# Kernel tuning notes

Measured on AMD Instinct MI355X. Metric: run time of the kernel, lower is better.

The kernel has to match this reference:

```python
import jax, jax.numpy as jnp
import numpy as np


def _gru(x, w_ih, w_hh, b_ih, b_hh):
    # x: [B, T, D]; torch nn.GRU (batch_first) semantics, h0 = 0
    B = x.shape[0]
    H = w_hh.shape[1]
    def step(h, xt):
        gi = xt @ w_ih.T + b_ih          # [B, 3H]
        gh = h @ w_hh.T + b_hh           # [B, 3H]
        ir, iz, inn = jnp.split(gi, 3, axis=-1)
        hr, hz, hn = jnp.split(gh, 3, axis=-1)
        r = jax.nn.sigmoid(ir + hr)
        z = jax.nn.sigmoid(iz + hz)
        n = jnp.tanh(inn + r * hn)
        h_new = (1.0 - z) * n + z * h
        return h_new, h_new
    h0 = jnp.zeros((B, H), x.dtype)
    _, ys = jax.lax.scan(step, h0, jnp.swapaxes(x, 0, 1))
    return jnp.swapaxes(ys, 0, 1)        # [B, T, H]


def setup_inputs() -> dict:
    key = jax.random.key(0)
    ks = iter(jax.random.split(key, 40))
    def p(shape, scale=0.05):
        return jax.random.normal(next(ks), shape, dtype=jnp.float32) * scale
    B, T, Z, S = 1024, 2, 100, 6
    return {
        "x": p((B, T, Z, S), 1.0),
        # actor: GRU(6 -> 64) + SimpleSubActor(64 -> 512 -> 128 -> 1)
        "a_gru_wih": p((192, 6)), "a_gru_whh": p((192, 64)),
        "a_gru_bih": p((192,)), "a_gru_bhh": p((192,)),
        "a_fc1_w": p((512, 64)), "a_fc1_b": p((512,)),
        "a_fc2_w": p((128, 512)), "a_fc2_b": p((128,)),
        "a_fc3_w": p((1, 128)), "a_fc3_b": p((1,)),
        # critic: GRU(35 -> 32) + SimpleSubCritic(32 -> 512 -> 256 -> 1)
        "c_gru_wih": p((96, 35)), "c_gru_whh": p((96, 32)),
        "c_gru_bih": p((96,)), "c_gru_bhh": p((96,)),
        "c_fc1_w": p((512, 32)), "c_fc1_b": p((512,)),
        "c_fc2_w": p((256, 512)), "c_fc2_b": p((256,)),
        "c_fc3_w": p((1, 256)), "c_fc3_b": p((1,)),
        # LocalizedModule(35 -> 512 -> 256 -> 1)
        "lm_fc1_w": p((512, 35)), "lm_fc1_b": p((512,)),
        "lm_fc2_w": p((256, 512)), "lm_fc2_b": p((256,)),
        "lm_fc3_w": p((1, 256)), "lm_fc3_b": p((1,)),
    }


def reference(x, a_gru_wih, a_gru_whh, a_gru_bih, a_gru_bhh,
              a_fc1_w, a_fc1_b, a_fc2_w, a_fc2_b, a_fc3_w, a_fc3_b,
              c_gru_wih, c_gru_whh, c_gru_bih, c_gru_bhh,
              c_fc1_w, c_fc1_b, c_fc2_w, c_fc2_b, c_fc3_w, c_fc3_b,
              lm_fc1_w, lm_fc1_b, lm_fc2_w, lm_fc2_b, lm_fc3_w, lm_fc3_b):
    B, T, Z, S = x.shape
    # ---- SimpleActor: same GRU+MLP shared across zones -> batch zones ----
    # torch: a[i] from x[:, :, i]; torch.stack(a) -> [Z, B, T, 1], then .view(-1, T, Z)
    xz = jnp.transpose(x, (2, 0, 1, 3)).reshape(Z * B, T, S)   # zones-major
    sx = _gru(xz, a_gru_wih, a_gru_whh, a_gru_bih, a_gru_bhh)  # [Z*B, T, 64]
    h = jax.nn.relu(sx @ a_fc1_w.T + a_fc1_b)
    h = jax.nn.relu(h @ a_fc2_w.T + a_fc2_b)
    sa = h @ a_fc3_w.T + a_fc3_b                               # [Z*B, T, 1]
    p = sa.reshape(-1, T, Z)                                   # faithful view(-1, t, nzones)
    # ---- concat action onto state ----
    xc = jnp.concatenate([x, p.reshape(-1, T, Z, 1)], axis=-1)  # [B, T, Z, 7]
    # ---- SimpleCritic: f/q lists reset each iter -> only zone i=99 survives ----
    # neighbors of 99: (99, 89, 100->zeros, 109->zeros, 98)
    zeros = jnp.zeros_like(xc[:, :, Z - 1])
    xi = jnp.concatenate([xc[:, :, 99], xc[:, :, 89], zeros, zeros, xc[:, :, 98]], axis=2)  # [B, T, 35]
    # LocalizedModule on last timestep
    hf = jax.nn.relu(xi[:, -1, :] @ lm_fc1_w.T + lm_fc1_b)
    hf = jax.nn.relu(hf @ lm_fc2_w.T + lm_fc2_b)
    f = hf @ lm_fc3_w.T + lm_fc3_b                             # [B, 1]
    # critic GRU + SimpleSubCritic (it keeps only last timestep)
    xq = _gru(xi, c_gru_wih, c_gru_whh, c_gru_bih, c_gru_bhh)  # [B, T, 32]
    hq = jax.nn.relu(xq[:, -1, :] @ c_fc1_w.T + c_fc1_b)
    hq = jax.nn.relu(hq @ c_fc2_w.T + c_fc2_b)
    qz = hq @ c_fc3_w.T + c_fc3_b                              # [B, 1]
    q = jnp.sum(f + qz, axis=1)                                # [B]
    return p[:, -1], q.reshape(-1, 1)
```

## Files before the change

kernel.cpp:

```cpp
#include <hip/hip_runtime.h>
#include <hip/hip_bf16.h>

#define NB 1024
#define NT 2
#define NZ 100
#define NS 6
#define NSEQ (NZ*NB)

typedef short short8 __attribute__((ext_vector_type(8)));
typedef float floatx4 __attribute__((ext_vector_type(4)));
typedef unsigned int uint2v __attribute__((ext_vector_type(2)));

__device__ __forceinline__ float sigm(float v)     { return 1.0f/(1.0f + __expf(-v)); }
__device__ __forceinline__ float tanhfast(float v) { float t = __expf(2.0f*v); return 1.0f - 2.0f/(t + 1.0f); }
__device__ __forceinline__ unsigned short f2bf(float f) {
    __hip_bfloat16 h = __float2bfloat16(f);
    return *reinterpret_cast<unsigned short*>(&h);
}

#define WS_WIHB   819200
#define WS_WHHB   (WS_WIHB + 192*32*2)
#define WS_W1B    (WS_WHHB + 192*64*2)
#define WS_W2B    (WS_W1B + 512*64*2)
#define WS_L1WB   (WS_W2B + 128*512*2)
#define WS_L2WB   (WS_L1WB + 512*64*2)
#define WS_CF1WB  (WS_L2WB + 256*512*2)
#define WS_CF2WB  (WS_CF1WB + 512*32*2)
#define WS_CWIHB  (WS_CF2WB + 256*512*2)
#define WS_CWHHB  (WS_CWIHB + 96*64*2)

#define PREP_N (116736 + 32768 + 131072 + 16384 + 131072 + 6144 + 3072)

__global__ __launch_bounds__(256)
void prep_kernel(const float* __restrict__ wih, const float* __restrict__ whh,
                 const float* __restrict__ w1,  const float* __restrict__ w2,
                 const float* __restrict__ l1w, const float* __restrict__ l2w,
                 const float* __restrict__ cf1w, const float* __restrict__ cf2w,
                 const float* __restrict__ cwih, const float* __restrict__ cwhh,
                 unsigned short* wihb, unsigned short* whhb,
                 unsigned short* w1b,  unsigned short* w2b,
                 unsigned short* l1wb, unsigned short* l2wb,
                 unsigned short* cf1wb, unsigned short* cf2wb,
                 unsigned short* cwihb, unsigned short* cwhhb)
{
    int e = blockIdx.x*256 + threadIdx.x;
    if (e < 6144) {
        int g = e >> 5, k = e & 31;
        wihb[e] = f2bf(k < 6 ? wih[g*6 + k] : 0.0f);
    } else if (e < 18432) {
        int i = e - 6144;  whhb[i] = f2bf(whh[i]);
    } else if (e < 51200) {
        int i = e - 18432; w1b[i] = f2bf(w1[i]);
    } else if (e < 116736) {
        int i = e - 51200; w2b[i] = f2bf(w2[i]);
    } else if (e < 149504) {
        int i = e - 116736; int o = i >> 6, k = i & 63;
        l1wb[i] = f2bf(k < 35 ? l1w[o*35 + k] : 0.0f);
    } else if (e < 280576) {
        int i = e - 149504; l2wb[i] = f2bf(l2w[i]);
    } else if (e < 296960) {
        int i = e - 280576; cf1wb[i] = f2bf(cf1w[i]);
    } else if (e < 428032) {
        int i = e - 296960; cf2wb[i] = f2bf(cf2w[i]);
    } else if (e < 434176) {
        int i = e - 428032; int o = i >> 6, k = i & 63;
        cwihb[i] = f2bf(k < 35 ? cwih[o*35 + k] : 0.0f);
    } else if (e < PREP_N) {
        int i = e - 434176; cwhhb[i] = f2bf(cwhh[i]);
    }
}

__device__ __forceinline__ short8 ldsfrag(const char* base, int rowstride, int r, int k0) {
    int byte = r*rowstride + k0*2;
    byte ^= ((r & 7) << 4);
    return *reinterpret_cast<const short8*>(base + byte);
}

__global__ __launch_bounds__(512, 4)
void actor_mfma(const float* __restrict__ x,
                const unsigned short* __restrict__ wihb, const unsigned short* __restrict__ whhb,
                const float* __restrict__ bih, const float* __restrict__ bhh,
                const unsigned short* __restrict__ w1b, const float* __restrict__ b1,
                const unsigned short* __restrict__ w2b, const float* __restrict__ b2,
                const float* __restrict__ w3, const float* __restrict__ b3,
                float* __restrict__ sa, float* __restrict__ out0)
{
    __shared__ __align__(16) char smem[40960];
    char*  sxb  = smem;
    float* fc3p = (float*)smem;
    char*  h1b  = smem + 8192;
    char*  xpad = smem + 8192;
    char*  h0b  = smem + 16384;

    const int tid  = threadIdx.x;
    const int wv   = tid >> 6;
    const int lane = tid & 63;
    const int r16  = lane & 15;
    const int g4   = lane >> 4;
    const int ft   = wv & 3;
    const int sq   = wv >> 2;
    const int s0   = blockIdx.x * 32;
    const int zz   = s0 >> 10;
    const int b0   = s0 & 1023;

    for (int e = tid; e < 1024; e += 512) {
        int row = e >> 4, j = e & 15;
        int t = row >> 5, sl = row & 31;
        unsigned int lo = 0, hi = 0;
        if (j < 2) {
            const float* xp = x + (((b0 + sl)*NT + t)*NZ + zz)*NS;
            int c0 = j*4;
            float v0 = xp[c0], v1 = xp[c0+1];
            float v2 = (c0+2 < 6) ? xp[c0+2] : 0.0f;
            float v3 = (c0+3 < 6) ? xp[c0+3] : 0.0f;
            lo = (unsigned int)f2bf(v0) | ((unsigned int)f2bf(v1) << 16);
            hi = (unsigned int)f2bf(v2) | ((unsigned int)f2bf(v3) << 16);
        }
        int byte = row*128 + j*8; byte ^= ((row & 7) << 4);
        uint2v vv = {lo, hi};
        *reinterpret_cast<uint2v*>(xpad + byte) = vv;
    }

    const int fb = ft*16 + g4*4;
    const floatx4 bihR = *reinterpret_cast<const floatx4*>(bih + fb);
    const floatx4 bihZ = *reinterpret_cast<const floatx4*>(bih + 64 + fb);
    const floatx4 bihN = *reinterpret_cast<const floatx4*>(bih + 128 + fb);
    const floatx4 bhhR = *reinterpret_cast<const floatx4*>(bhh + fb);
    const floatx4 bhhZ = *reinterpret_cast<const floatx4*>(bhh + 64 + fb);
    const floatx4 bhhN = *reinterpret_cast<const floatx4*>(bhh + 128 + fb);
    __syncthreads();

    floatx4 h0;
    {
        short8 bx = ldsfrag(xpad, 128, sq*16 + r16, g4*8);
        const short8 aR = *reinterpret_cast<const short8*>(wihb + ((ft     )*16 + r16)*32 + g4*8);
        const short8 aZ = *reinterpret_cast<const short8*>(wihb + ((ft +  4)*16 + r16)*32 + g4*8);
        const short8 aN = *reinterpret_cast<const short8*>(wihb + ((ft +  8)*16 + r16)*32 + g4*8);
        floatx4 gR = {0,0,0,0}, gZ = {0,0,0,0}, gN = {0,0,0,0};
        gR = __builtin_amdgcn_mfma_f32_16x16x32_bf16(aR, bx, gR, 0, 0, 0);
        gZ = __builtin_amdgcn_mfma_f32_16x16x32_bf16(aZ, bx, gZ, 0, 0, 0);
        gN = __builtin_amdgcn_mfma_f32_16x16x32_bf16(aN, bx, gN, 0, 0, 0);
        #pragma unroll
        for (int q = 0; q < 4; ++q) {
            float r = sigm(gR[q] + bihR[q] + bhhR[q]);
            float z = sigm(gZ[q] + bihZ[q] + bhhZ[q]);
            float n = tanhfast(gN[q] + bihN[q] + r*bhhN[q]);
            h0[q] = (1.0f - z)*n;
        }
        unsigned int lo = (unsigned int)f2bf(h0[0]) | ((unsigned int)f2bf(h0[1]) << 16);
        unsigned int hi = (unsigned int)f2bf(h0[2]) | ((unsigned int)f2bf(h0[3]) << 16);
        uint2v vv = {lo, hi};
        int seq = sq*16 + r16;
        int b1a = seq*128 + fb*2; b1a ^= ((seq & 7) << 4);
        *reinterpret_cast<uint2v*>(h0b + b1a) = vv;
        *reinterpret_cast<uint2v*>(sxb + b1a) = vv;
    }

    floatx4 gR1 = {0,0,0,0}, gZ1 = {0,0,0,0}, gN1 = {0,0,0,0};
    {
        short8 bx = ldsfrag(xpad, 128, 32 + sq*16 + r16, g4*8);
        const short8 aR = *reinterpret_cast<const short8*>(wihb + ((ft     )*16 + r16)*32 + g4*8);
        const short8 aZ = *reinterpret_cast<const short8*>(wihb + ((ft +  4)*16 + r16)*32 + g4*8);
        const short8 aN = *reinterpret_cast<const short8*>(wihb + ((ft +  8)*16 + r16)*32 + g4*8);
        gR1 = __builtin_amdgcn_mfma_f32_16x16x32_bf16(aR, bx, gR1, 0, 0, 0);
        gZ1 = __builtin_amdgcn_mfma_f32_16x16x32_bf16(aZ, bx, gZ1, 0, 0, 0);
        gN1 = __builtin_amdgcn_mfma_f32_16x16x32_bf16(aN, bx, gN1, 0, 0, 0);
    }
    __syncthreads();

    {
        short8 bh0 = ldsfrag(h0b, 128, sq*16 + r16, g4*8);
        short8 bh1 = ldsfrag(h0b, 128, sq*16 + r16, 32 + g4*8);
        floatx4 hR = {0,0,0,0}, hZ = {0,0,0,0}, hN = {0,0,0,0};
        #pragma unroll
        for (int p = 0; p < 2; ++p) {
            short8 bh = p ? bh1 : bh0;
            const short8 aR = *reinterpret_cast<const short8*>(whhb + ((ft     )*16 + r16)*64 + p*32 + g4*8);
            const short8 aZ = *reinterpret_cast<const short8*>(whhb + ((ft +  4)*16 + r16)*64 + p*32 + g4*8);
            const short8 aN = *reinterpret_cast<const short8*>(whhb + ((ft +  8)*16 + r16)*64 + p*32 + g4*8);
            hR = __builtin_amdgcn_mfma_f32_16x16x32_bf16(aR, bh, hR, 0, 0, 0);
            hZ = __builtin_amdgcn_mfma_f32_16x16x32_bf16(aZ, bh, hZ, 0, 0, 0);
            hN = __builtin_amdgcn_mfma_f32_16x16x32_bf16(aN, bh, hN, 0, 0, 0);
        }
        floatx4 hn;
        #pragma unroll
        for (int q = 0; q < 4; ++q) {
            float r = sigm(gR1[q] + bihR[q] + hR[q] + bhhR[q]);
            float z = sigm(gZ1[q] + bihZ[q] + hZ[q] + bhhZ[q]);
            float n = tanhfast(gN1[q] + bihN[q] + r*(hN[q] + bhhN[q]));
            hn[q] = (1.0f - z)*n + z*h0[q];
        }
        unsigned int lo = (unsigned int)f2bf(hn[0]) | ((unsigned int)f2bf(hn[1]) << 16);
        unsigned int hi = (unsigned int)f2bf(hn[2]) | ((unsigned int)f2bf(hn[3]) << 16);
        uint2v vv = {lo, hi};
        int row = 32 + sq*16 + r16;
        int ba = row*128 + fb*2; ba ^= ((row & 7) << 4);
        *reinterpret_cast<uint2v*>(sxb + ba) = vv;
    }
    __syncthreads();

    floatx4 acc[4];
    {
        const floatx4 bias2 = *reinterpret_cast<const floatx4*>(b2 + wv*16 + g4*4);
        #pragma unroll
        for (int rt = 0; rt < 4; ++rt) acc[rt] = bias2;
    }

    #pragma unroll
    for (int h = 0; h < 2; ++h) {
        #pragma unroll
        for (int rt = 0; rt < 4; ++rt) {
            short8 f0 = ldsfrag(sxb, 128, rt*16 + r16, g4*8);
            short8 f1 = ldsfrag(sxb, 128, rt*16 + r16, 32 + g4*8);
            #pragma unroll
            for (int j = 0; j < 2; ++j) {
                int mtg = h*16 + wv*2 + j;
                int mtl = wv*2 + j;
                const short8 a0 = *reinterpret_cast<const short8*>(w1b + (mtg*16 + r16)*64 + g4*8);
                const short8 a1 = *reinterpret_cast<const short8*>(w1b + (mtg*16 + r16)*64 + 32 + g4*8);
                floatx4 a = *reinterpret_cast<const floatx4*>(b1 + mtg*16 + g4*4);
                a = __builtin_amdgcn_mfma_f32_16x16x32_bf16(a0, f0, a, 0, 0, 0);
                a = __builtin_amdgcn_mfma_f32_16x16x32_bf16(a1, f1, a, 0, 0, 0);
                unsigned int lo = (unsigned int)f2bf(fmaxf(a[0],0.f)) | ((unsigned int)f2bf(fmaxf(a[1],0.f)) << 16);
                unsigned int hi = (unsigned int)f2bf(fmaxf(a[2],0.f)) | ((unsigned int)f2bf(fmaxf(a[3],0.f)) << 16);
                int row = rt*16 + r16;
                int byte = row*512 + (mtl*16 + g4*4)*2; byte ^= ((row & 7) << 4);
                uint2v vv = {lo, hi};
                *reinterpret_cast<uint2v*>(h1b + byte) = vv;
            }
        }
        __syncthreads();

        {
            const unsigned short* wp = w2b + (wv*16 + r16)*512 + h*256 + g4*8;
            #pragma unroll
            for (int ks = 0; ks < 8; ++ks) {
                const short8 a = *reinterpret_cast<const short8*>(wp + ks*32);
                #pragma unroll
                for (int rt = 0; rt < 4; ++rt) {
                    short8 bb = ldsfrag(h1b, 512, rt*16 + r16, ks*32 + g4*8);
                    acc[rt] = __builtin_amdgcn_mfma_f32_16x16x32_bf16(a, bb, acc[rt], 0, 0, 0);
                }
            }
        }
        __syncthreads();
    }

    {
        const floatx4 w3v = *reinterpret_cast<const floatx4*>(w3 + wv*16 + g4*4);
        #pragma unroll
        for (int rt = 0; rt < 4; ++rt) {
            float p = fmaxf(acc[rt][0],0.f)*w3v[0] + fmaxf(acc[rt][1],0.f)*w3v[1]
                    + fmaxf(acc[rt][2],0.f)*w3v[2] + fmaxf(acc[rt][3],0.f)*w3v[3];
            p += __shfl_xor(p, 16);
            p += __shfl_xor(p, 32);
            if (g4 == 0) fc3p[wv*64 + rt*16 + r16] = p;
        }
    }
    __syncthreads();

    if (tid < 64) {
        float v = b3[0];
        #pragma unroll
        for (int w = 0; w < 8; ++w) v += fc3p[w*64 + tid];
        int t = tid >> 5, sl = tid & 31;
        int gseq = s0 + sl;
        int i = gseq*2 + t;
        sa[i] = v;
        int m = i % 200;
        if (m >= 100) out0[(i/200)*NZ + (m - 100)] = v;
    }
}

__global__ __launch_bounds__(512)
void critic_mfma(const float* __restrict__ x, const float* __restrict__ sa,
                 const unsigned short* __restrict__ cwihb, const unsigned short* __restrict__ cwhhb,
                 const float* __restrict__ cbih, const float* __restrict__ cbhh,
                 const unsigned short* __restrict__ cf1wb, const float* __restrict__ cf1b,
                 const unsigned short* __restrict__ cf2wb, const float* __restrict__ cf2b,
                 const float* __restrict__ cf3w, const float* __restrict__ cf3b,
                 const unsigned short* __restrict__ l1wb, const float* __restrict__ l1b,
                 const unsigned short* __restrict__ l2wb, const float* __restrict__ l2b,
                 const float* __restrict__ l3w, const float* __restrict__ l3b,
                 float* __restrict__ outq)
{
    __shared__ __align__(16) char smem[25600];
    char*  xib = smem;
    char*  h1b = smem + 4096;
    char*  h0b = smem + 20480;
    char*  hqb = smem + 22528;
    float* fp  = (float*)(smem + 24576);
    float* qp  = (float*)(smem + 25088);

    const int tid  = threadIdx.x;
    const int wv   = tid >> 6;
    const int lane = tid & 63;
    const int r16  = lane & 15;
    const int g4   = lane >> 4;
    const int b0   = blockIdx.x * 16;

    for (int e = tid; e < 2048; e += 512) {
        int trow = e >> 6, k = e & 63;
        int t = trow >> 4, row = trow & 15;
        int b = b0 + row;
        float v = 0.0f;
        if (k < 35) {
            int slot = k / 7, s = k - slot*7;
            int nb = (slot==0)?99:((slot==1)?89:((slot==4)?98:-1));
            if (nb >= 0) v = (s < 6) ? x[((b*NT + t)*NZ + nb)*NS + s]
                                     : sa[b*200 + t*100 + nb];
        }
        int byte = trow*128 + k*2; byte ^= ((trow & 7) << 4);
        *reinterpret_cast<unsigned short*>(xib + byte) = f2bf(v);
    }
    __syncthreads();

    {
        short8 bx0 = ldsfrag(xib, 128, 16 + r16, g4*8);
        short8 bx1 = ldsfrag(xib, 128, 16 + r16, 32 + g4*8);
        #pragma unroll
        for (int j = 0; j < 4; ++j) {
            int mt = wv*4 + j;
            const short8 a0 = *reinterpret_cast<const short8*>(l1wb + (mt*16 + r16)*64 + g4*8);
            const short8 a1 = *reinterpret_cast<const short8*>(l1wb + (mt*16 + r16)*64 + 32 + g4*8);
            floatx4 acc = *reinterpret_cast<const floatx4*>(l1b + mt*16 + g4*4);
            acc = __builtin_amdgcn_mfma_f32_16x16x32_bf16(a0, bx0, acc, 0, 0, 0);
            acc = __builtin_amdgcn_mfma_f32_16x16x32_bf16(a1, bx1, acc, 0, 0, 0);
            unsigned int lo = (unsigned int)f2bf(fmaxf(acc[0],0.f)) | ((unsigned int)f2bf(fmaxf(acc[1],0.f)) << 16);
            unsigned int hi = (unsigned int)f2bf(fmaxf(acc[2],0.f)) | ((unsigned int)f2bf(fmaxf(acc[3],0.f)) << 16);
            int byte = r16*1024 + (mt*16 + g4*4)*2; byte ^= ((r16 & 7) << 4);
            uint2v vv = {lo, hi};
            *reinterpret_cast<uint2v*>(h1b + byte) = vv;
        }
    }
    __syncthreads();

    {
        int mt0 = wv*2, mt1 = wv*2 + 1;
        floatx4 acc0 = *reinterpret_cast<const floatx4*>(l2b + mt0*16 + g4*4);
        floatx4 acc1 = *reinterpret_cast<const floatx4*>(l2b + mt1*16 + g4*4);
        const unsigned short* wp0 = l2wb + (mt0*16 + r16)*512 + g4*8;
        const unsigned short* wp1 = l2wb + (mt1*16 + r16)*512 + g4*8;
        for (int ks = 0; ks < 16; ++ks) {
            short8 bb = ldsfrag(h1b, 1024, r16, ks*32 + g4*8);
            const short8 a0 = *reinterpret_cast<const short8*>(wp0 + ks*32);
            const short8 a1 = *reinterpret_cast<const short8*>(wp1 + ks*32);
            acc0 = __builtin_amdgcn_mfma_f32_16x16x32_bf16(a0, bb, acc0, 0, 0, 0);
            acc1 = __builtin_amdgcn_mfma_f32_16x16x32_bf16(a1, bb, acc1, 0, 0, 0);
        }
        const floatx4 w0 = *reinterpret_cast<const floatx4*>(l3w + mt0*16 + g4*4);
        const floatx4 w1 = *reinterpret_cast<const floatx4*>(l3w + mt1*16 + g4*4);
        float p = fmaxf(acc0[0],0.f)*w0[0] + fmaxf(acc0[1],0.f)*w0[1]
                + fmaxf(acc0[2],0.f)*w0[2] + fmaxf(acc0[3],0.f)*w0[3]
                + fmaxf(acc1[0],0.f)*w1[0] + fmaxf(acc1[1],0.f)*w1[1]
                + fmaxf(acc1[2],0.f)*w1[2] + fmaxf(acc1[3],0.f)*w1[3];
        p += __shfl_xor(p, 16);
        p += __shfl_xor(p, 32);
        if (g4 == 0) fp[wv*16 + r16] = p;
    }
    __syncthreads();

    floatx4 h0r = {0,0,0,0};
    floatx4 gR1 = {0,0,0,0}, gZ1 = {0,0,0,0}, gN1 = {0,0,0,0};
    floatx4 bihR, bihZ, bihN, bhhR, bhhZ, bhhN;
    if (wv < 2) {
        const int hf = wv;
        const int fb = hf*16 + g4*4;
        bihR = *reinterpret_cast<const floatx4*>(cbih + fb);
        bihZ = *reinterpret_cast<const floatx4*>(cbih + 32 + fb);
        bihN = *reinterpret_cast<const floatx4*>(cbih + 64 + fb);
        bhhR = *reinterpret_cast<const floatx4*>(cbhh + fb);
        bhhZ = *reinterpret_cast<const floatx4*>(cbhh + 32 + fb);
        bhhN = *reinterpret_cast<const floatx4*>(cbhh + 64 + fb);
        short8 bx0 = ldsfrag(xib, 128, r16, g4*8);
        short8 bx1 = ldsfrag(xib, 128, r16, 32 + g4*8);
        short8 cx0 = ldsfrag(xib, 128, 16 + r16, g4*8);
        short8 cx1 = ldsfrag(xib, 128, 16 + r16, 32 + g4*8);
        floatx4 gR0 = {0,0,0,0}, gZ0 = {0,0,0,0}, gN0 = {0,0,0,0};
        #pragma unroll
        for (int p = 0; p < 2; ++p) {
            const short8 aR = *reinterpret_cast<const short8*>(cwihb + ((hf    )*16 + r16)*64 + p*32 + g4*8);
            const short8 aZ = *reinterpret_cast<const short8*>(cwihb + ((2+hf  )*16 + r16)*64 + p*32 + g4*8);
            const short8 aN = *reinterpret_cast<const short8*>(cwihb + ((4+hf  )*16 + r16)*64 + p*32 + g4*8);
            short8 b0f = p ? bx1 : bx0;
            short8 b1f = p ? cx1 : cx0;
            gR0 = __builtin_amdgcn_mfma_f32_16x16x32_bf16(aR, b0f, gR0, 0, 0, 0);
            gZ0 = __builtin_amdgcn_mfma_f32_16x16x32_bf16(aZ, b0f, gZ0, 0, 0, 0);
            gN0 = __builtin_amdgcn_mfma_f32_16x16x32_bf16(aN, b0f, gN0, 0, 0, 0);
            gR1 = __builtin_amdgcn_mfma_f32_16x16x32_bf16(aR, b1f, gR1, 0, 0, 0);
            gZ1 = __builtin_amdgcn_mfma_f32_16x16x32_bf16(aZ, b1f, gZ1, 0, 0, 0);
            gN1 = __builtin_amdgcn_mfma_f32_16x16x32_bf16(aN, b1f, gN1, 0, 0, 0);
        }
        #pragma unroll
        for (int q = 0; q < 4; ++q) {
            float r = sigm(gR0[q] + bihR[q] + bhhR[q]);
            float z = sigm(gZ0[q] + bihZ[q] + bhhZ[q]);
            float n = tanhfast(gN0[q] + bihN[q] + r*bhhN[q]);
            h0r[q] = (1.0f - z)*n;
        }
        unsigned int lo = (unsigned int)f2bf(h0r[0]) | ((unsigned int)f2bf(h0r[1]) << 16);
        unsigned int hi = (unsigned int)f2bf(h0r[2]) | ((unsigned int)f2bf(h0r[3]) << 16);
        uint2v vv = {lo, hi};
        int byte = r16*128 + fb*2; byte ^= ((r16 & 7) << 4);
        *reinterpret_cast<uint2v*>(h0b + byte) = vv;
    }
    __syncthreads();
    if (wv < 2) {
        const int hf = wv;
        const int fb = hf*16 + g4*4;
        short8 bh = ldsfrag(h0b, 128, r16, g4*8);
        const short8 aR = *reinterpret_cast<const short8*>(cwhhb + ((hf    )*16 + r16)*32 + g4*8);
        const short8 aZ = *reinterpret_cast<const short8*>(cwhhb + ((2+hf  )*16 + r16)*32 + g4*8);
        const short8 aN = *reinterpret_cast<const short8*>(cwhhb + ((4+hf  )*16 + r16)*32 + g4*8);
        floatx4 hR = {0,0,0,0}, hZ = {0,0,0,0}, hN = {0,0,0,0};
        hR = __builtin_amdgcn_mfma_f32_16x16x32_bf16(aR, bh, hR, 0, 0, 0);
        hZ = __builtin_amdgcn_mfma_f32_16x16x32_bf16(aZ, bh, hZ, 0, 0, 0);
        hN = __builtin_amdgcn_mfma_f32_16x16x32_bf16(aN, bh, hN, 0, 0, 0);
        floatx4 hn;
        #pragma unroll
        for (int q = 0; q < 4; ++q) {
            float r = sigm(gR1[q] + bihR[q] + hR[q] + bhhR[q]);
            float z = sigm(gZ1[q] + bihZ[q] + hZ[q] + bhhZ[q]);
            float n = tanhfast(gN1[q] + bihN[q] + r*(hN[q] + bhhN[q]));
            hn[q] = (1.0f - z)*n + z*h0r[q];
        }
        unsigned int lo = (unsigned int)f2bf(hn[0]) | ((unsigned int)f2bf(hn[1]) << 16);
        unsigned int hi = (unsigned int)f2bf(hn[2]) | ((unsigned int)f2bf(hn[3]) << 16);
        uint2v vv = {lo, hi};
        int byte = r16*128 + fb*2; byte ^= ((r16 & 7) << 4);
        *reinterpret_cast<uint2v*>(hqb + byte) = vv;
    }
    __syncthreads();

    {
        short8 bq = ldsfrag(hqb, 128, r16, g4*8);
        #pragma unroll
        for (int j = 0; j < 4; ++j) {
            int mt = wv*4 + j;
            const short8 a = *reinterpret_cast<const short8*>(cf1wb + (mt*16 + r16)*32 + g4*8);
            floatx4 acc = *reinterpret_cast<const floatx4*>(cf1b + mt*16 + g4*4);
            acc = __builtin_amdgcn_mfma_f32_16x16x32_bf16(a, bq, acc, 0, 0, 0);
            unsigned int lo = (unsigned int)f2bf(fmaxf(acc[0],0.f)) | ((unsigned int)f2bf(fmaxf(acc[1],0.f)) << 16);
            unsigned int hi = (unsigned int)f2bf(fmaxf(acc[2],0.f)) | ((unsigned int)f2bf(fmaxf(acc[3],0.f)) << 16);
            int byte = r16*1024 + (mt*16 + g4*4)*2; byte ^= ((r16 & 7) << 4);
            uint2v vv = {lo, hi};
            *reinterpret_cast<uint2v*>(h1b + byte) = vv;
        }
    }
    __syncthreads();

    {
        int mt0 = wv*2, mt1 = wv*2 + 1;
        floatx4 acc0 = *reinterpret_cast<const floatx4*>(cf2b + mt0*16 + g4*4);
        floatx4 acc1 = *reinterpret_cast<const floatx4*>(cf2b + mt1*16 + g4*4);
        const unsigned short* wp0 = cf2wb + (mt0*16 + r16)*512 + g4*8;
        const unsigned short* wp1 = cf2wb + (mt1*16 + r16)*512 + g4*8;
        for (int ks = 0; ks < 16; ++ks) {
            short8 bb = ldsfrag(h1b, 1024, r16, ks*32 + g4*8);
            const short8 a0 = *reinterpret_cast<const short8*>(wp0 + ks*32);
            const short8 a1 = *reinterpret_cast<const short8*>(wp1 + ks*32);
            acc0 = __builtin_amdgcn_mfma_f32_16x16x32_bf16(a0, bb, acc0, 0, 0, 0);
            acc1 = __builtin_amdgcn_mfma_f32_16x16x32_bf16(a1, bb, acc1, 0, 0, 0);
        }
        const floatx4 w0 = *reinterpret_cast<const floatx4*>(cf3w + mt0*16 + g4*4);
        const floatx4 w1 = *reinterpret_cast<const floatx4*>(cf3w + mt1*16 + g4*4);
        float p = fmaxf(acc0[0],0.f)*w0[0] + fmaxf(acc0[1],0.f)*w0[1]
                + fmaxf(acc0[2],0.f)*w0[2] + fmaxf(acc0[3],0.f)*w0[3]
                + fmaxf(acc1[0],0.f)*w1[0] + fmaxf(acc1[1],0.f)*w1[1]
                + fmaxf(acc1[2],0.f)*w1[2] + fmaxf(acc1[3],0.f)*w1[3];
        p += __shfl_xor(p, 16);
        p += __shfl_xor(p, 32);
        if (g4 == 0) qp[wv*16 + r16] = p;
    }
    __syncthreads();

    if (tid < 16) {
        float f = l3b[0], qz = cf3b[0];
        #pragma unroll
        for (int w = 0; w < 8; ++w) { f += fp[w*16 + tid]; qz += qp[w*16 + tid]; }
        outq[b0 + tid] = f + qz;
    }
}

extern "C" void kernel_launch(void* const* d_in, const int* in_sizes, int n_in,
                              void* d_out, int out_size, void* d_ws, size_t ws_size,
                              hipStream_t stream)
{
    (void)in_sizes; (void)n_in; (void)out_size; (void)ws_size;
    const float* x     = (const float*)d_in[0];
    const float* a_wih = (const float*)d_in[1];
    const float* a_whh = (const float*)d_in[2];
    const float* a_bih = (const float*)d_in[3];
    const float* a_bhh = (const float*)d_in[4];
    const float* a1w   = (const float*)d_in[5];
    const float* a1b   = (const float*)d_in[6];
    const float* a2w   = (const float*)d_in[7];
    const float* a2b   = (const float*)d_in[8];
    const float* a3w   = (const float*)d_in[9];
    const float* a3b   = (const float*)d_in[10];
    const float* cwih  = (const float*)d_in[11];
    const float* cwhh  = (const float*)d_in[12];
    const float* cbih  = (const float*)d_in[13];
    const float* cbhh  = (const float*)d_in[14];
    const float* cf1w  = (const float*)d_in[15];
    const float* cf1b  = (const float*)d_in[16];
    const float* cf2w  = (const float*)d_in[17];
    const float* cf2b  = (const float*)d_in[18];
    const float* cf3w  = (const float*)d_in[19];
    const float* cf3b  = (const float*)d_in[20];
    const float* l1w   = (const float*)d_in[21];
    const float* l1b   = (const float*)d_in[22];
    const float* l2w   = (const float*)d_in[23];
    const float* l2b   = (const float*)d_in[24];
    const float* l3w   = (const float*)d_in[25];
    const float* l3b   = (const float*)d_in[26];

    float* sa = (float*)d_ws;
    unsigned short* wihb  = (unsigned short*)((char*)d_ws + WS_WIHB);
    unsigned short* whhb  = (unsigned short*)((char*)d_ws + WS_WHHB);
    unsigned short* w1b   = (unsigned short*)((char*)d_ws + WS_W1B);
    unsigned short* w2b   = (unsigned short*)((char*)d_ws + WS_W2B);
    unsigned short* l1wb  = (unsigned short*)((char*)d_ws + WS_L1WB);
    unsigned short* l2wb  = (unsigned short*)((char*)d_ws + WS_L2WB);
    unsigned short* cf1wb = (unsigned short*)((char*)d_ws + WS_CF1WB);
    unsigned short* cf2wb = (unsigned short*)((char*)d_ws + WS_CF2WB);
    unsigned short* cwihb = (unsigned short*)((char*)d_ws + WS_CWIHB);
    unsigned short* cwhhb = (unsigned short*)((char*)d_ws + WS_CWHHB);
    float* out0 = (float*)d_out;
    float* outq = (float*)d_out + NB*NZ;

    hipLaunchKernelGGL(prep_kernel, dim3((PREP_N + 255)/256), dim3(256), 0, stream,
                       a_wih, a_whh, a1w, a2w, l1w, l2w, cf1w, cf2w, cwih, cwhh,
                       wihb, whhb, w1b, w2b, l1wb, l2wb, cf1wb, cf2wb, cwihb, cwhhb);
    hipLaunchKernelGGL(actor_mfma, dim3(NSEQ/32), dim3(512), 0, stream,
                       x, wihb, whhb, a_bih, a_bhh, w1b, a1b, w2b, a2b, a3w, a3b, sa, out0);
    hipLaunchKernelGGL(critic_mfma, dim3(NB/16), dim3(512), 0, stream,
                       x, sa, cwihb, cwhhb, cbih, cbhh, cf1wb, cf1b, cf2wb, cf2b, cf3w, cf3b,
                       l1wb, l1b, l2wb, l2b, l3w, l3b, outq);
}
```

Measured before the change: 160.5 us.

## Process 64 sequences per actor block and load x directly into MFMA fragments

The actor kernel now handles 64 sequences per block instead of 32, so each wave covers two sequence tiles and reuses its GRU and FC weight fragments across twice as many rows; the grid is halved. The LDS staging of x is removed: each lane loads its six input floats straight from global memory into a bf16 fragment, which also drops a barrier. The recurrent weight fragments are hoisted out of the per-tile loop. The cost is 80 KB of LDS per block and doubled accumulator registers, which likely lowers the number of resident blocks per CU.

```diff
diff --git a/kernel.cpp b/kernel.cpp
--- a/kernel.cpp
+++ b/kernel.cpp
@@ -76,6 +76,18 @@
     return *reinterpret_cast<const short8*>(base + byte);
 }
 
+__device__ __forceinline__ short8 xfrag(const float* __restrict__ xp) {
+    float2 a  = *reinterpret_cast<const float2*>(xp);
+    float2 b2 = *reinterpret_cast<const float2*>(xp + 2);
+    float2 c  = *reinterpret_cast<const float2*>(xp + 4);
+    short8 f;
+    f[0] = (short)f2bf(a.x);  f[1] = (short)f2bf(a.y);
+    f[2] = (short)f2bf(b2.x); f[3] = (short)f2bf(b2.y);
+    f[4] = (short)f2bf(c.x);  f[5] = (short)f2bf(c.y);
+    f[6] = 0; f[7] = 0;
+    return f;
+}
+
 __global__ __launch_bounds__(512, 4)
 void actor_mfma(const float* __restrict__ x,
                 const unsigned short* __restrict__ wihb, const unsigned short* __restrict__ whhb,
@@ -85,11 +97,10 @@
                 const float* __restrict__ w3, const float* __restrict__ b3,
                 float* __restrict__ sa, float* __restrict__ out0)
 {
-    __shared__ __align__(16) char smem[40960];
+    __shared__ __align__(16) char smem[81920];
     char*  sxb  = smem;
     float* fc3p = (float*)smem;
-    char*  h1b  = smem + 8192;
-    char*  xpad = smem + 8192;
+    char*  h1b  = smem + 16384;
     char*  h0b  = smem + 16384;
 
     const int tid  = threadIdx.x;
@@ -99,27 +110,9 @@
     const int g4   = lane >> 4;
     const int ft   = wv & 3;
     const int sq   = wv >> 2;
-    const int s0   = blockIdx.x * 32;
+    const int s0   = blockIdx.x * 64;
     const int zz   = s0 >> 10;
     const int b0   = s0 & 1023;
-
-    for (int e = tid; e < 1024; e += 512) {
-        int row = e >> 4, j = e & 15;
-        int t = row >> 5, sl = row & 31;
-        unsigned int lo = 0, hi = 0;
-        if (j < 2) {
-            const float* xp = x + (((b0 + sl)*NT + t)*NZ + zz)*NS;
-            int c0 = j*4;
-            float v0 = xp[c0], v1 = xp[c0+1];
-            float v2 = (c0+2 < 6) ? xp[c0+2] : 0.0f;
-            float v3 = (c0+3 < 6) ? xp[c0+3] : 0.0f;
-            lo = (unsigned int)f2bf(v0) | ((unsigned int)f2bf(v1) << 16);
-            hi = (unsigned int)f2bf(v2) | ((unsigned int)f2bf(v3) << 16);
-        }
-        int byte = row*128 + j*8; byte ^= ((row & 7) << 4);
-        uint2v vv = {lo, hi};
-        *reinterpret_cast<uint2v*>(xpad + byte) = vv;
-    }
 
     const int fb = ft*16 + g4*4;
     const floatx4 bihR = *reinterpret_cast<const floatx4*>(bih + fb);
@@ -128,88 +121,99 @@
     const floatx4 bhhR = *reinterpret_cast<const floatx4*>(bhh + fb);
     const floatx4 bhhZ = *reinterpret_cast<const floatx4*>(bhh + 64 + fb);
     const floatx4 bhhN = *reinterpret_cast<const floatx4*>(bhh + 128 + fb);
-    __syncthreads();
-
-    floatx4 h0;
-    {
-        short8 bx = ldsfrag(xpad, 128, sq*16 + r16, g4*8);
+
+    floatx4 h0[2];
+    floatx4 g1R[2], g1Z[2], g1N[2];
+
+    {
         const short8 aR = *reinterpret_cast<const short8*>(wihb + ((ft     )*16 + r16)*32 + g4*8);
         const short8 aZ = *reinterpret_cast<const short8*>(wihb + ((ft +  4)*16 + r16)*32 + g4*8);
         const short8 aN = *reinterpret_cast<const short8*>(wihb + ((ft +  8)*16 + r16)*32 + g4*8);
-        floatx4 gR = {0,0,0,0}, gZ = {0,0,0,0}, gN = {0,0,0,0};
-        gR = __builtin_amdgcn_mfma_f32_16x16x32_bf16(aR, bx, gR, 0, 0, 0);
-        gZ = __builtin_amdgcn_mfma_f32_16x16x32_bf16(aZ, bx, gZ, 0, 0, 0);
-        gN = __builtin_amdgcn_mfma_f32_16x16x32_bf16(aN, bx, gN, 0, 0, 0);
-        #pragma unroll
-        for (int q = 0; q < 4; ++q) {
-            float r = sigm(gR[q] + bihR[q] + bhhR[q]);
-            float z = sigm(gZ[q] + bihZ[q] + bhhZ[q]);
-            float n = tanhfast(gN[q] + bihN[q] + r*bhhN[q]);
-            h0[q] = (1.0f - z)*n;
-        }
-        unsigned int lo = (unsigned int)f2bf(h0[0]) | ((unsigned int)f2bf(h0[1]) << 16);
-        unsigned int hi = (unsigned int)f2bf(h0[2]) | ((unsigned int)f2bf(h0[3]) << 16);
-        uint2v vv = {lo, hi};
-        int seq = sq*16 + r16;
-        int b1a = seq*128 + fb*2; b1a ^= ((seq & 7) << 4);
-        *reinterpret_cast<uint2v*>(h0b + b1a) = vv;
-        *reinterpret_cast<uint2v*>(sxb + b1a) = vv;
-    }
-
-    floatx4 gR1 = {0,0,0,0}, gZ1 = {0,0,0,0}, gN1 = {0,0,0,0};
-    {
-        short8 bx = ldsfrag(xpad, 128, 32 + sq*16 + r16, g4*8);
-        const short8 aR = *reinterpret_cast<const short8*>(wihb + ((ft     )*16 + r16)*32 + g4*8);
-        const short8 aZ = *reinterpret_cast<const short8*>(wihb + ((ft +  4)*16 + r16)*32 + g4*8);
-        const short8 aN = *reinterpret_cast<const short8*>(wihb + ((ft +  8)*16 + r16)*32 + g4*8);
-        gR1 = __builtin_amdgcn_mfma_f32_16x16x32_bf16(aR, bx, gR1, 0, 0, 0);
-        gZ1 = __builtin_amdgcn_mfma_f32_16x16x32_bf16(aZ, bx, gZ1, 0, 0, 0);
-        gN1 = __builtin_amdgcn_mfma_f32_16x16x32_bf16(aN, bx, gN1, 0, 0, 0);
-    }
-    __syncthreads();
-
-    {
-        short8 bh0 = ldsfrag(h0b, 128, sq*16 + r16, g4*8);
-        short8 bh1 = ldsfrag(h0b, 128, sq*16 + r16, 32 + g4*8);
-        floatx4 hR = {0,0,0,0}, hZ = {0,0,0,0}, hN = {0,0,0,0};
-        #pragma unroll
-        for (int p = 0; p < 2; ++p) {
-            short8 bh = p ? bh1 : bh0;
-            const short8 aR = *reinterpret_cast<const short8*>(whhb + ((ft     )*16 + r16)*64 + p*32 + g4*8);
-            const short8 aZ = *reinterpret_cast<const short8*>(whhb + ((ft +  4)*16 + r16)*64 + p*32 + g4*8);
-            const short8 aN = *reinterpret_cast<const short8*>(whhb + ((ft +  8)*16 + r16)*64 + p*32 + g4*8);
-            hR = __builtin_amdgcn_mfma_f32_16x16x32_bf16(aR, bh, hR, 0, 0, 0);
-            hZ = __builtin_amdgcn_mfma_f32_16x16x32_bf16(aZ, bh, hZ, 0, 0, 0);
-            hN = __builtin_amdgcn_mfma_f32_16x16x32_bf16(aN, bh, hN, 0, 0, 0);
-        }
-        floatx4 hn;
-        #pragma unroll
-        for (int q = 0; q < 4; ++q) {
-            float r = sigm(gR1[q] + bihR[q] + hR[q] + bhhR[q]);
-            float z = sigm(gZ1[q] + bihZ[q] + hZ[q] + bhhZ[q]);
-            float n = tanhfast(gN1[q] + bihN[q] + r*(hN[q] + bhhN[q]));
-            hn[q] = (1.0f - z)*n + z*h0[q];
-        }
-        unsigned int lo = (unsigned int)f2bf(hn[0]) | ((unsigned int)f2bf(hn[1]) << 16);
-        unsigned int hi = (unsigned int)f2bf(hn[2]) | ((unsigned int)f2bf(hn[3]) << 16);
-        uint2v vv = {lo, hi};
-        int row = 32 + sq*16 + r16;
-        int ba = row*128 + fb*2; ba ^= ((row & 7) << 4);
-        *reinterpret_cast<uint2v*>(sxb + ba) = vv;
-    }
-    __syncthreads();
-
-    floatx4 acc[4];
+        #pragma unroll
+        for (int u = 0; u < 2; ++u) {
+            const int st  = sq*2 + u;
+            const int seq = st*16 + r16;
+            const int b   = b0 + seq;
+            const float* xrow = x + ((b*NT)*NZ + zz)*NS;
+            short8 bx0 = xfrag(xrow);
+            short8 bx1 = xfrag(xrow + NZ*NS);
+            floatx4 gR = {0,0,0,0}, gZ = {0,0,0,0}, gN = {0,0,0,0};
+            gR = __builtin_amdgcn_mfma_f32_16x16x32_bf16(aR, bx0, gR, 0, 0, 0);
+            gZ = __builtin_amdgcn_mfma_f32_16x16x32_bf16(aZ, bx0, gZ, 0, 0, 0);
+            gN = __builtin_amdgcn_mfma_f32_16x16x32_bf16(aN, bx0, gN, 0, 0, 0);
+            floatx4 t1R = {0,0,0,0}, t1Z = {0,0,0,0}, t1N = {0,0,0,0};
+            t1R = __builtin_amdgcn_mfma_f32_16x16x32_bf16(aR, bx1, t1R, 0, 0, 0);
+            t1Z = __builtin_amdgcn_mfma_f32_16x16x32_bf16(aZ, bx1, t1Z, 0, 0, 0);
+            t1N = __builtin_amdgcn_mfma_f32_16x16x32_bf16(aN, bx1, t1N, 0, 0, 0);
+            g1R[u] = t1R; g1Z[u] = t1Z; g1N[u] = t1N;
+            floatx4 hh;
+            #pragma unroll
+            for (int q = 0; q < 4; ++q) {
+                float r = sigm(gR[q] + bihR[q] + bhhR[q]);
+                float z = sigm(gZ[q] + bihZ[q] + bhhZ[q]);
+                float n = tanhfast(gN[q] + bihN[q] + r*bhhN[q]);
+                hh[q] = (1.0f - z)*n;
+            }
+            h0[u] = hh;
+            unsigned int lo = (unsigned int)f2bf(hh[0]) | ((unsigned int)f2bf(hh[1]) << 16);
+            unsigned int hi = (unsigned int)f2bf(hh[2]) | ((unsigned int)f2bf(hh[3]) << 16);
+            uint2v vv = {lo, hi};
+            int ba = seq*128 + fb*2; ba ^= ((seq & 7) << 4);
+            *reinterpret_cast<uint2v*>(h0b + ba) = vv;
+            *reinterpret_cast<uint2v*>(sxb + ba) = vv;
+        }
+    }
+    __syncthreads();
+
+    {
+        const short8 wR0 = *reinterpret_cast<const short8*>(whhb + ((ft     )*16 + r16)*64 + g4*8);
+        const short8 wR1 = *reinterpret_cast<const short8*>(whhb + ((ft     )*16 + r16)*64 + 32 + g4*8);
+        const short8 wZ0 = *reinterpret_cast<const short8*>(whhb + ((ft +  4)*16 + r16)*64 + g4*8);
+        const short8 wZ1 = *reinterpret_cast<const short8*>(whhb + ((ft +  4)*16 + r16)*64 + 32 + g4*8);
+        const short8 wN0 = *reinterpret_cast<const short8*>(whhb + ((ft +  8)*16 + r16)*64 + g4*8);
+        const short8 wN1 = *reinterpret_cast<const short8*>(whhb + ((ft +  8)*16 + r16)*64 + 32 + g4*8);
+        #pragma unroll
+        for (int u = 0; u < 2; ++u) {
+            const int st  = sq*2 + u;
+            const int seq = st*16 + r16;
+            short8 bh0 = ldsfrag(h0b, 128, seq, g4*8);
+            short8 bh1 = ldsfrag(h0b, 128, seq, 32 + g4*8);
+            floatx4 hR = {0,0,0,0}, hZ = {0,0,0,0}, hN = {0,0,0,0};
+            hR = __builtin_amdgcn_mfma_f32_16x16x32_bf16(wR0, bh0, hR, 0, 0, 0);
+            hZ = __builtin_amdgcn_mfma_f32_16x16x32_bf16(wZ0, bh0, hZ, 0, 0, 0);
+            hN = __builtin_amdgcn_mfma_f32_16x16x32_bf16(wN0, bh0, hN, 0, 0, 0);
+            hR = __builtin_amdgcn_mfma_f32_16x16x32_bf16(wR1, bh1, hR, 0, 0, 0);
+            hZ = __builtin_amdgcn_mfma_f32_16x16x32_bf16(wZ1, bh1, hZ, 0, 0, 0);
+            hN = __builtin_amdgcn_mfma_f32_16x16x32_bf16(wN1, bh1, hN, 0, 0, 0);
+            floatx4 hn;
+            #pragma unroll
+            for (int q = 0; q < 4; ++q) {
+                float r = sigm(g1R[u][q] + bihR[q] + hR[q] + bhhR[q]);
+                float z = sigm(g1Z[u][q] + bihZ[q] + hZ[q] + bhhZ[q]);
+                float n = tanhfast(g1N[u][q] + bihN[q] + r*(hN[q] + bhhN[q]));
+                hn[q] = (1.0f - z)*n + z*h0[u][q];
+            }
+            unsigned int lo = (unsigned int)f2bf(hn[0]) | ((unsigned int)f2bf(hn[1]) << 16);
+            unsigned int hi = (unsigned int)f2bf(hn[2]) | ((unsigned int)f2bf(hn[3]) << 16);
+            uint2v vv = {lo, hi};
+            int row = 64 + seq;
+            int ba = row*128 + fb*2; ba ^= ((row & 7) << 4);
+            *reinterpret_cast<uint2v*>(sxb + ba) = vv;
+        }
+    }
+    __syncthreads();
+
+    floatx4 acc[8];
     {
         const floatx4 bias2 = *reinterpret_cast<const floatx4*>(b2 + wv*16 + g4*4);
         #pragma unroll
-        for (int rt = 0; rt < 4; ++rt) acc[rt] = bias2;
+        for (int rt = 0; rt < 8; ++rt) acc[rt] = bias2;
     }
 
     #pragma unroll
     for (int h = 0; h < 2; ++h) {
         #pragma unroll
-        for (int rt = 0; rt < 4; ++rt) {
+        for (int rt = 0; rt < 8; ++rt) {
             short8 f0 = ldsfrag(sxb, 128, rt*16 + r16, g4*8);
             short8 f1 = ldsfrag(sxb, 128, rt*16 + r16, 32 + g4*8);
             #pragma unroll
@@ -237,7 +241,7 @@
             for (int ks = 0; ks < 8; ++ks) {
                 const short8 a = *reinterpret_cast<const short8*>(wp + ks*32);
                 #pragma unroll
-                for (int rt = 0; rt < 4; ++rt) {
+                for (int rt = 0; rt < 8; ++rt) {
                     short8 bb = ldsfrag(h1b, 512, rt*16 + r16, ks*32 + g4*8);
                     acc[rt] = __builtin_amdgcn_mfma_f32_16x16x32_bf16(a, bb, acc[rt], 0, 0, 0);
                 }
@@ -249,21 +253,21 @@
     {
         const floatx4 w3v = *reinterpret_cast<const floatx4*>(w3 + wv*16 + g4*4);
         #pragma unroll
-        for (int rt = 0; rt < 4; ++rt) {
+        for (int rt = 0; rt < 8; ++rt) {
             float p = fmaxf(acc[rt][0],0.f)*w3v[0] + fmaxf(acc[rt][1],0.f)*w3v[1]
                     + fmaxf(acc[rt][2],0.f)*w3v[2] + fmaxf(acc[rt][3],0.f)*w3v[3];
             p += __shfl_xor(p, 16);
             p += __shfl_xor(p, 32);
-            if (g4 == 0) fc3p[wv*64 + rt*16 + r16] = p;
-        }
-    }
-    __syncthreads();
-
-    if (tid < 64) {
+            if (g4 == 0) fc3p[wv*128 + rt*16 + r16] = p;
+        }
+    }
+    __syncthreads();
+
+    if (tid < 128) {
         float v = b3[0];
         #pragma unroll
-        for (int w = 0; w < 8; ++w) v += fc3p[w*64 + tid];
-        int t = tid >> 5, sl = tid & 31;
+        for (int w = 0; w < 8; ++w) v += fc3p[w*128 + tid];
+        int t = tid >> 6, sl = tid & 63;
         int gseq = s0 + sl;
         int i = gseq*2 + t;
         sa[i] = v;
@@ -532,7 +536,7 @@
     hipLaunchKernelGGL(prep_kernel, dim3((PREP_N + 255)/256), dim3(256), 0, stream,
                        a_wih, a_whh, a1w, a2w, l1w, l2w, cf1w, cf2w, cwih, cwhh,
                        wihb, whhb, w1b, w2b, l1wb, l2wb, cf1wb, cf2wb, cwihb, cwhhb);
-    hipLaunchKernelGGL(actor_mfma, dim3(NSEQ/32), dim3(512), 0, stream,
+    hipLaunchKernelGGL(actor_mfma, dim3(NSEQ/64), dim3(512), 0, stream,
                        x, wihb, whhb, a_bih, a_bhh, w1b, a1b, w2b, a2b, a3w, a3b, sa, out0);
     hipLaunchKernelGGL(critic_mfma, dim3(NB/16), dim3(512), 0, stream,
                        x, sa, cwihb, cwhhb, cbih, cbhh, cf1wb, cf1b, cf2wb, cf2b, cf3w, cf3b,
```

After: 187.2 us. +16.6%, slower.
